# Optimization experiments

Measured on AMD Instinct MI355X. Metric: run time of the kernel, lower is better.

Reference implementation:

```python
import jax, jax.numpy as jnp
import numpy as np

B, T_OUT, L, D, H = 1, 8, 512, 512, 8  # batch, frames, tokens/frame, d_model, heads


def setup_inputs() -> dict:
    key = jax.random.key(0)
    ks = jax.random.split(key, 7)
    return {
        "hidden_states": jax.random.normal(ks[0], (B * T_OUT, L, D), jnp.float32),
        "p_out": jax.random.normal(ks[1], (B, T_OUT, 4, 4), jnp.float32),
        "p_out_inv": jax.random.normal(ks[2], (B, T_OUT, 4, 4), jnp.float32),
        "Wq": jax.random.normal(ks[3], (D, D), jnp.float32) * 0.02,
        "Wk": jax.random.normal(ks[4], (D, D), jnp.float32) * 0.02,
        "Wv": jax.random.normal(ks[5], (D, D), jnp.float32) * 0.02,
        "Wo": jax.random.normal(ks[6], (D, D), jnp.float32) * 0.02,
        "bo": jnp.zeros((D,), jnp.float32),
        "num_heads": H,
    }


def cape_embed(f, P):
    # f: (b, S, d), P: (b, S, 4, 4); rearrange '(d k)'->'d k' with k=4, matmul by P, flatten back
    b, S, d = f.shape
    f4 = f.reshape(b, S, d // 4, 4)
    return jnp.einsum('bsdk,bskg->bsdg', f4, P).reshape(b, S, d)


def reference(hidden_states, p_out, p_out_inv, Wq, Wk, Wv, Wo, bo, num_heads):
    b, t_out = p_out.shape[0], p_out.shape[1]
    bt, l, d = hidden_states.shape
    S = t_out * l
    residual = hidden_states

    # '(b t_out) l d -> b (t_out l) d'
    x = hidden_states.reshape(b, S, d)

    q = x @ Wq
    k = x @ Wk
    v = x @ Wv

    # repeat per-frame CAPE matrices over tokens within each frame; self-attn so p_in = p_out
    Pq = jnp.repeat(p_out_inv, l, axis=1)  # (b, S, 4, 4)
    Pk = jnp.repeat(p_out, l, axis=1)      # (b, S, 4, 4)
    q = cape_embed(q, Pq)
    k = cape_embed(k, Pk)

    hd = d // num_heads
    scale = hd ** -0.5
    qh = q.reshape(b, S, num_heads, hd).transpose(0, 2, 1, 3)  # (b, h, S, hd)
    kh = k.reshape(b, S, num_heads, hd).transpose(0, 2, 1, 3)
    vh = v.reshape(b, S, num_heads, hd).transpose(0, 2, 1, 3)

    scores = jnp.einsum('bhqd,bhkd->bhqk', qh, kh) * scale  # full (b,h,S,S) matrix
    probs = jax.nn.softmax(scores, axis=-1)
    o = jnp.einsum('bhqk,bhkd->bhqd', probs, vh)

    o = o.transpose(0, 2, 1, 3).reshape(b, S, d)
    o = o @ Wo + bo  # to_out[0]; to_out[1] dropout is identity in eval

    # 'b (t_out l) d -> (b t_out) l d'
    o = o.reshape(bt, l, d)
    return o + residual  # residual_connection; rescale_output_factor = 1.0
```

## Files before the change

### kernel.cpp

```cpp
#include <hip/hip_runtime.h>
#include <hip/hip_bf16.h>
#include <stdint.h>

typedef __bf16 bf16_t;
typedef __bf16 bf16x2 __attribute__((ext_vector_type(2)));
typedef __bf16 bf16x4 __attribute__((ext_vector_type(4)));
typedef __bf16 bf16x8 __attribute__((ext_vector_type(8)));
typedef float f32x4 __attribute__((ext_vector_type(4)));

#define MFMA(a, b, c) __builtin_amdgcn_mfma_f32_16x16x32_bf16(a, b, c, 0, 0, 0)

#if __has_builtin(__builtin_amdgcn_exp2f)
#define FEXP2 __builtin_amdgcn_exp2f
#else
#define FEXP2 exp2f
#endif

__device__ __forceinline__ void g2lds16(const void* g, void* l) {
  __builtin_amdgcn_global_load_lds(
      reinterpret_cast<const __attribute__((address_space(1))) unsigned int*>(
          reinterpret_cast<uintptr_t>(g)),
      reinterpret_cast<__attribute__((address_space(3))) unsigned int*>(
          reinterpret_cast<uintptr_t>(l)),
      16, 0, 0);
}

__device__ __forceinline__ unsigned cvtpk(float lo, float hi) {
  unsigned r;
  asm("v_cvt_pk_bf16_f32 %0, %1, %2" : "=v"(r) : "v"(lo), "v"(hi));
  return r;
}

__device__ __forceinline__ void lane_swap32(unsigned& a, unsigned& b) {
#if __has_builtin(__builtin_amdgcn_permlane32_swap)
  typedef int i32x2 __attribute__((ext_vector_type(2)));
  i32x2 r = __builtin_amdgcn_permlane32_swap((int)a, (int)b, false, false);
  a = (unsigned)r[0];
  b = (unsigned)r[1];
#else
  asm("v_permlane32_swap_b32 %0, %1" : "+v"(a), "+v"(b));
#endif
}

__device__ __forceinline__ void lane_swap16(unsigned& a, unsigned& b) {
#if __has_builtin(__builtin_amdgcn_permlane16_swap)
  typedef int i32x2 __attribute__((ext_vector_type(2)));
  i32x2 r = __builtin_amdgcn_permlane16_swap((int)a, (int)b, false, false);
  a = (unsigned)r[0];
  b = (unsigned)r[1];
#else
  asm("v_permlane16_swap_b32 %0, %1" : "+v"(a), "+v"(b));
#endif
}

__global__ __launch_bounds__(256) void k_prep(const float* __restrict__ x,
                                              const float* __restrict__ Wq,
                                              const float* __restrict__ Wk,
                                              const float* __restrict__ Wv,
                                              const float* __restrict__ Wo,
                                              const float* __restrict__ Pout,
                                              const float* __restrict__ Pinv,
                                              bf16_t* __restrict__ Xbf,
                                              bf16_t* __restrict__ WqT,
                                              bf16_t* __restrict__ WkT,
                                              bf16_t* __restrict__ WvT,
                                              bf16_t* __restrict__ WoT) {
  const int bid = blockIdx.x;
  if (bid < 2048) {
    int i = (bid * 256 + threadIdx.x) * 4;
    float4 v = *reinterpret_cast<const float4*>(x + i);
    bf16x4 o;
    o[0] = (bf16_t)v.x; o[1] = (bf16_t)v.y; o[2] = (bf16_t)v.z; o[3] = (bf16_t)v.w;
    *reinterpret_cast<bf16x4*>(Xbf + i) = o;
  } else if (bid < 3072) {
    int idx = (bid - 2048) * 256 + threadIdx.x;
    int t = idx >> 15;
    int n = (idx >> 6) & 511;
    int k0 = (idx & 63) << 3;
    int dq4 = (n >> 2) << 2;
    int g = n & 3;
    float pq[4], pk[4];
#pragma unroll
    for (int h = 0; h < 4; ++h) {
      pq[h] = Pinv[t * 16 + h * 4 + g];
      pk[h] = Pout[t * 16 + h * 4 + g];
    }
    bf16x8 oq, ok;
#pragma unroll
    for (int j = 0; j < 8; ++j) {
      const float4 wq = *reinterpret_cast<const float4*>(Wq + (size_t)(k0 + j) * 512 + dq4);
      const float4 wk = *reinterpret_cast<const float4*>(Wk + (size_t)(k0 + j) * 512 + dq4);
      oq[j] = (bf16_t)((wq.x * pq[0] + wq.y * pq[1] + wq.z * pq[2] + wq.w * pq[3]) * 0.1803368801f);
      ok[j] = (bf16_t)(wk.x * pk[0] + wk.y * pk[1] + wk.z * pk[2] + wk.w * pk[3]);
    }
    size_t o = ((size_t)t * 512 + n) * 512 + k0;
    *reinterpret_cast<bf16x8*>(WqT + o) = oq;
    *reinterpret_cast<bf16x8*>(WkT + o) = ok;
  } else {
    int idx = (bid - 3072) * 256 + threadIdx.x;
    int mat = idx >> 15;
    int n = (idx >> 6) & 511;
    int k0 = (idx & 63) << 3;
    const float* W = mat ? Wo : Wv;
    bf16_t* T = mat ? WoT : WvT;
    bf16x8 o;
#pragma unroll
    for (int j = 0; j < 8; ++j) o[j] = (bf16_t)W[(size_t)(k0 + j) * 512 + n];
    *reinterpret_cast<bf16x8*>(T + (size_t)n * 512 + k0) = o;
  }
}

__global__ __launch_bounds__(256) void k_gemm_qkv(const bf16_t* __restrict__ Xbf,
                                                  const bf16_t* __restrict__ WqT,
                                                  const bf16_t* __restrict__ WkT,
                                                  const bf16_t* __restrict__ WvT,
                                                  bf16_t* __restrict__ Qh,
                                                  bf16_t* __restrict__ Kh,
                                                  bf16_t* __restrict__ Vt) {
  __shared__ bf16_t lA[128 * 64];
  __shared__ bf16_t lB[64 * 64];
  const int m0 = blockIdx.x * 128, n0 = blockIdx.y * 64;
  const int mat = blockIdx.z;
  const int frame = m0 >> 9;
  const bf16_t* WT = (mat == 0) ? (WqT + (size_t)frame * 512 * 512)
                   : (mat == 1) ? (WkT + (size_t)frame * 512 * 512)
                                : WvT;
  const int tid = threadIdx.x, lane = tid & 63, wid = tid >> 6;
  const int wr = wid >> 1, wc = wid & 1;
  const int l15 = lane & 15, lg = lane >> 4;
  const int srow = lane >> 3;
  const int scol = ((lane & 7) ^ (lane >> 3)) << 3;

  f32x4 acc[4][2] = {};

  for (int kt = 0; kt < 512; kt += 64) {
#pragma unroll
    for (int i = 0; i < 4; ++i) {
      int chunk = wid * 4 + i;
      int row = chunk * 8 + srow;
      g2lds16(Xbf + (size_t)(m0 + row) * 512 + kt + scol, lA + chunk * 512);
    }
#pragma unroll
    for (int i = 0; i < 2; ++i) {
      int chunk = wid * 2 + i;
      int row = chunk * 8 + srow;
      g2lds16(WT + (size_t)(n0 + row) * 512 + kt + scol, lB + chunk * 512);
    }
    __syncthreads();
#pragma unroll
    for (int kk = 0; kk < 2; ++kk) {
      bf16x8 af[4], bw[2];
      int c16 = ((4 * kk + lg) ^ (l15 & 7)) << 3;
#pragma unroll
      for (int i = 0; i < 4; ++i)
        af[i] = *reinterpret_cast<const bf16x8*>(lA + (wr * 64 + i * 16 + l15) * 64 + c16);
#pragma unroll
      for (int j = 0; j < 2; ++j)
        bw[j] = *reinterpret_cast<const bf16x8*>(lB + (wc * 32 + j * 16 + l15) * 64 + c16);
#pragma unroll
      for (int i = 0; i < 4; ++i)
#pragma unroll
        for (int j = 0; j < 2; ++j)
          acc[i][j] = MFMA(af[i], bw[j], acc[i][j]);
    }
    __syncthreads();
  }

#pragma unroll
  for (int i = 0; i < 4; ++i)
#pragma unroll
    for (int j = 0; j < 2; ++j)
#pragma unroll
      for (int r = 0; r < 4; ++r) {
        int s = m0 + wr * 64 + i * 16 + lg * 4 + r;
        int n = n0 + wc * 32 + j * 16 + l15;
        bf16_t v = (bf16_t)acc[i][j][r];
        if (mat == 2) {
          Vt[(size_t)n * 4096 + s] = v;
        } else if (mat == 0) {
          Qh[((size_t)(n >> 6) * 4096 + s) * 64 + (n & 63)] = v;
        } else {
          Kh[((size_t)(n >> 6) * 4096 + s) * 64 + (n & 63)] = v;
        }
      }
}

__global__ __launch_bounds__(256, 2) void k_attn(const bf16_t* __restrict__ Qh,
                                                 const bf16_t* __restrict__ Kh,
                                                 const bf16_t* __restrict__ Vt,
                                                 char* __restrict__ wsb,
                                                 float* __restrict__ Lp) {
  __shared__ bf16_t lK[2][64 * 64];
  __shared__ bf16_t lV[2][64 * 64];
  const int h = blockIdx.y;
  const int ks = blockIdx.z;
  const int q0 = blockIdx.x * 256;
  const int tid = threadIdx.x, lane = tid & 63, wid = tid >> 6;
  const int l15 = lane & 15, lg = lane >> 4;
  const int srow = lane >> 3;
  const int scol = ((lane & 7) ^ (lane >> 3)) << 3;

  bf16_t* Op = (bf16_t*)(ks < 3 ? wsb + ((size_t)ks << 22) : wsb + (29u << 20));

  bf16x8 qf[4][2];
#pragma unroll
  for (int g = 0; g < 4; ++g) {
    const bf16_t* Qp = Qh + ((size_t)h * 4096 + q0 + wid * 64 + g * 16 + l15) * 64;
#pragma unroll
    for (int kk = 0; kk < 2; ++kk)
      qf[g][kk] = *reinterpret_cast<const bf16x8*>(Qp + kk * 32 + lg * 8);
  }

  bf16x8 onesf;
#pragma unroll
  for (int j = 0; j < 8; ++j) onesf[j] = (bf16_t)1.0f;

  const bf16_t* Kb = Kh + ((size_t)h * 4096 + ks * 1024) * 64;
  const bf16_t* Vb = Vt + (size_t)h * 64 * 4096 + ks * 1024;

  f32x4 oT[4][4] = {};
  f32x4 lac[4] = {};

  auto stage = [&](int buf, int kt) {
#pragma unroll
    for (int i = 0; i < 2; ++i) {
      int chunk = wid * 2 + i;
      int row = chunk * 8 + srow;
      g2lds16(Kb + (size_t)(kt + row) * 64 + scol, &lK[buf][chunk * 512]);
      g2lds16(Vb + (size_t)row * 4096 + kt + scol, &lV[buf][chunk * 512]);
    }
  };

  stage(0, 0);
  __syncthreads();

  for (int t = 0; t < 16; ++t) {
    const int cur = t & 1;
    if (t < 15) stage(cur ^ 1, (t + 1) * 64);

    f32x4 st[4][4] = {};
    __builtin_amdgcn_s_setprio(1);
#pragma unroll
    for (int kk = 0; kk < 2; ++kk)
#pragma unroll
      for (int mb = 0; mb < 4; ++mb) {
        bf16x8 kf = *reinterpret_cast<const bf16x8*>(
            &lK[cur][(mb * 16 + l15) * 64 + (((kk * 4 + lg) ^ (l15 & 7)) << 3)]);
        st[0][mb] = MFMA(kf, qf[0][kk], st[0][mb]);
        st[1][mb] = MFMA(kf, qf[1][kk], st[1][mb]);
        st[2][mb] = MFMA(kf, qf[2][kk], st[2][mb]);
        st[3][mb] = MFMA(kf, qf[3][kk], st[3][mb]);
      }
    __builtin_amdgcn_s_setprio(0);

#pragma unroll
    for (int g = 0; g < 4; ++g)
#pragma unroll
      for (int mb = 0; mb < 4; ++mb)
#pragma unroll
        for (int r = 0; r < 4; ++r)
          st[g][mb][r] = FEXP2(st[g][mb][r]);

    bf16x8 pb[4][2];
#pragma unroll
    for (int g = 0; g < 4; ++g)
#pragma unroll
      for (int kk = 0; kk < 2; ++kk) {
        unsigned A  = cvtpk(st[g][2 * kk][0],     st[g][2 * kk][1]);
        unsigned Ap = cvtpk(st[g][2 * kk][2],     st[g][2 * kk][3]);
        unsigned B  = cvtpk(st[g][2 * kk + 1][0], st[g][2 * kk + 1][1]);
        unsigned Bp = cvtpk(st[g][2 * kk + 1][2], st[g][2 * kk + 1][3]);
        lane_swap32(A, B);
        lane_swap16(A, B);
        lane_swap32(Ap, Bp);
        lane_swap16(Ap, Bp);
        union { unsigned u[4]; bf16x8 v; } pu;
        pu.u[0] = A; pu.u[1] = Ap; pu.u[2] = B; pu.u[3] = Bp;
        pb[g][kk] = pu.v;
      }

    __builtin_amdgcn_s_setprio(1);
#pragma unroll
    for (int kk = 0; kk < 2; ++kk) {
      lac[0] = MFMA(onesf, pb[0][kk], lac[0]);
      lac[1] = MFMA(onesf, pb[1][kk], lac[1]);
      lac[2] = MFMA(onesf, pb[2][kk], lac[2]);
      lac[3] = MFMA(onesf, pb[3][kk], lac[3]);
#pragma unroll
      for (int hb = 0; hb < 4; ++hb) {
        bf16x8 vf = *reinterpret_cast<const bf16x8*>(
            &lV[cur][(hb * 16 + l15) * 64 + (((kk * 4 + lg) ^ (l15 & 7)) << 3)]);
        oT[0][hb] = MFMA(vf, pb[0][kk], oT[0][hb]);
        oT[1][hb] = MFMA(vf, pb[1][kk], oT[1][hb]);
        oT[2][hb] = MFMA(vf, pb[2][kk], oT[2][hb]);
        oT[3][hb] = MFMA(vf, pb[3][kk], oT[3][hb]);
      }
    }
    __builtin_amdgcn_s_setprio(0);
    __syncthreads();
  }

#pragma unroll
  for (int g = 0; g < 4; ++g) {
    int q = q0 + wid * 64 + g * 16 + l15;
    size_t rbase = ((size_t)ks * 8 + h) * 4096 + q;
    size_t obase = ((size_t)h * 4096 + q) * 64;
    if (lg == 0) Lp[rbase] = lac[g][0];
#pragma unroll
    for (int hb = 0; hb < 4; ++hb) {
      bf16x4 ov;
#pragma unroll
      for (int r = 0; r < 4; ++r) ov[r] = (bf16_t)oT[g][hb][r];
      *reinterpret_cast<bf16x4*>(Op + obase + hb * 16 + lg * 4) = ov;
    }
  }
}

__global__ __launch_bounds__(256) void k_merge(char* __restrict__ wsb,
                                               const float* __restrict__ Lp,
                                               bf16_t* __restrict__ Obf) {
  int idx = blockIdx.x * 256 + threadIdx.x;
  int d4 = (idx & 15) << 2;
  int row = idx >> 4;
  float l = 0.f;
  f32x4 o = {};
#pragma unroll
  for (int s = 0; s < 4; ++s) {
    const bf16_t* Ops = (const bf16_t*)(s < 3 ? wsb + ((size_t)s << 22) : wsb + (29u << 20));
    l += Lp[s * 32768 + row];
    bf16x4 v = *reinterpret_cast<const bf16x4*>(Ops + (size_t)row * 64 + d4);
    o[0] += (float)v[0]; o[1] += (float)v[1];
    o[2] += (float)v[2]; o[3] += (float)v[3];
  }
  float rinv = 1.f / l;
  int h = row >> 12, q = row & 4095;
  bf16x4 ov;
#pragma unroll
  for (int r = 0; r < 4; ++r) ov[r] = (bf16_t)(o[r] * rinv);
  *reinterpret_cast<bf16x4*>(Obf + (size_t)q * 512 + h * 64 + d4) = ov;
}

__global__ __launch_bounds__(256) void k_gemm_out(const bf16_t* __restrict__ Obf,
                                                  const bf16_t* __restrict__ WoT,
                                                  const float* __restrict__ bo,
                                                  const float* __restrict__ resid,
                                                  float* __restrict__ out) {
  __shared__ bf16_t lA[64 * 64];
  __shared__ bf16_t lB[64 * 64];
  const int m0 = blockIdx.x * 64, n0 = blockIdx.y * 64;
  const int tid = threadIdx.x, lane = tid & 63, wid = tid >> 6;
  const int wr = wid >> 1, wc = wid & 1;
  const int l15 = lane & 15, lg = lane >> 4;
  const int srow = lane >> 3;
  const int scol = ((lane & 7) ^ (lane >> 3)) << 3;

  f32x4 acc[2][2] = {};

  for (int kt = 0; kt < 512; kt += 64) {
#pragma unroll
    for (int i = 0; i < 2; ++i) {
      int chunk = wid * 2 + i;
      int row = chunk * 8 + srow;
      g2lds16(Obf + (size_t)(m0 + row) * 512 + kt + scol, lA + chunk * 512);
      g2lds16(WoT + (size_t)(n0 + row) * 512 + kt + scol, lB + chunk * 512);
    }
    __syncthreads();
#pragma unroll
    for (int kk = 0; kk < 2; ++kk) {
      bf16x8 af[2], bw[2];
      int c16 = ((4 * kk + lg) ^ (l15 & 7)) << 3;
#pragma unroll
      for (int i = 0; i < 2; ++i) {
        af[i] = *reinterpret_cast<const bf16x8*>(lA + (wr * 32 + i * 16 + l15) * 64 + c16);
        bw[i] = *reinterpret_cast<const bf16x8*>(lB + (wc * 32 + i * 16 + l15) * 64 + c16);
      }
#pragma unroll
      for (int i = 0; i < 2; ++i)
#pragma unroll
        for (int j = 0; j < 2; ++j)
          acc[i][j] = MFMA(af[i], bw[j], acc[i][j]);
    }
    __syncthreads();
  }

#pragma unroll
  for (int i = 0; i < 2; ++i)
#pragma unroll
    for (int j = 0; j < 2; ++j)
#pragma unroll
      for (int r = 0; r < 4; ++r) {
        int s = m0 + wr * 32 + i * 16 + lg * 4 + r;
        int n = n0 + wc * 32 + j * 16 + l15;
        size_t o = (size_t)s * 512 + n;
        out[o] = acc[i][j][r] + bo[n] + resid[o];
      }
}

extern "C" void kernel_launch(void* const* d_in, const int* in_sizes, int n_in,
                              void* d_out, int out_size, void* d_ws, size_t ws_size,
                              hipStream_t stream) {
  const float* hs   = (const float*)d_in[0];
  const float* pout = (const float*)d_in[1];
  const float* pinv = (const float*)d_in[2];
  const float* Wq   = (const float*)d_in[3];
  const float* Wk   = (const float*)d_in[4];
  const float* Wv   = (const float*)d_in[5];
  const float* Wo   = (const float*)d_in[6];
  const float* bo   = (const float*)d_in[7];
  float* out = (float*)d_out;

  char* ws = (char*)d_ws;
  bf16_t* Xbf = (bf16_t*)(ws);
  bf16_t* WqT = (bf16_t*)(ws + (4u << 20));
  bf16_t* WkT = (bf16_t*)(ws + (8u << 20));
  bf16_t* WvT = (bf16_t*)(ws + (12u << 20));
  bf16_t* WoT = (bf16_t*)(ws + (12u << 20) + (512u << 10));
  bf16_t* Qh  = (bf16_t*)(ws + (13u << 20));
  bf16_t* Kh  = (bf16_t*)(ws + (17u << 20));
  bf16_t* Vt  = (bf16_t*)(ws + (21u << 20));
  bf16_t* Obf = (bf16_t*)(ws + (25u << 20));
  float*  Lp  = (float*)(ws + (33u << 20));

  hipLaunchKernelGGL(k_prep, dim3(3328), dim3(256), 0, stream,
                     hs, Wq, Wk, Wv, Wo, pout, pinv, Xbf, WqT, WkT, WvT, WoT);
  hipLaunchKernelGGL(k_gemm_qkv, dim3(32, 8, 3), dim3(256), 0, stream,
                     Xbf, WqT, WkT, WvT, Qh, Kh, Vt);
  hipLaunchKernelGGL(k_attn, dim3(16, 8, 4), dim3(256), 0, stream, Qh, Kh, Vt, ws, Lp);
  hipLaunchKernelGGL(k_merge, dim3(2048), dim3(256), 0, stream, ws, Lp, Obf);
  hipLaunchKernelGGL(k_gemm_out, dim3(64, 8), dim3(256), 0, stream, Obf, WoT, bo, hs, out);
}
```

Before: 93.76 us.

## Fuse split-K attention merge into output GEMM and widen QKV GEMM tile

Removes the separate k_merge kernel. The output-projection GEMM now sums the four split-K partial outputs, normalizes them by the summed row sums, and writes the merged bf16 A tile straight into LDS, so the Obf round trip and one launch go away. The QKV GEMM tile grows from 128x64 to 128x128, which halves the grid and improves per-block operand reuse. The trade-off is that each of the 8 column blocks of the out GEMM recomputes the merge for its rows, giving redundant partial-O reads. The larger QKV tile also gives fewer blocks, which may fill the CUs less evenly.

```diff
diff --git a/kernel.cpp b/kernel.cpp
--- a/kernel.cpp
+++ b/kernel.cpp
@@ -118,8 +118,8 @@
                                                   bf16_t* __restrict__ Kh,
                                                   bf16_t* __restrict__ Vt) {
   __shared__ bf16_t lA[128 * 64];
-  __shared__ bf16_t lB[64 * 64];
-  const int m0 = blockIdx.x * 128, n0 = blockIdx.y * 64;
+  __shared__ bf16_t lB[128 * 64];
+  const int m0 = blockIdx.x * 128, n0 = blockIdx.y * 128;
   const int mat = blockIdx.z;
   const int frame = m0 >> 9;
   const bf16_t* WT = (mat == 0) ? (WqT + (size_t)frame * 512 * 512)
@@ -131,7 +131,7 @@
   const int srow = lane >> 3;
   const int scol = ((lane & 7) ^ (lane >> 3)) << 3;
 
-  f32x4 acc[4][2] = {};
+  f32x4 acc[4][4] = {};
 
   for (int kt = 0; kt < 512; kt += 64) {
 #pragma unroll
@@ -139,28 +139,24 @@
       int chunk = wid * 4 + i;
       int row = chunk * 8 + srow;
       g2lds16(Xbf + (size_t)(m0 + row) * 512 + kt + scol, lA + chunk * 512);
-    }
-#pragma unroll
-    for (int i = 0; i < 2; ++i) {
-      int chunk = wid * 2 + i;
-      int row = chunk * 8 + srow;
       g2lds16(WT + (size_t)(n0 + row) * 512 + kt + scol, lB + chunk * 512);
     }
     __syncthreads();
 #pragma unroll
     for (int kk = 0; kk < 2; ++kk) {
-      bf16x8 af[4], bw[2];
-      int c16 = ((4 * kk + lg) ^ (l15 & 7)) << 3;
+      bf16x8 af[4], bw[4];
+#pragma unroll
+      for (int i = 0; i < 4; ++i) {
+        int ar = wr * 64 + i * 16 + l15;
+        int br = wc * 64 + i * 16 + l15;
+        int c16 = ((4 * kk + lg) ^ (l15 & 7)) << 3;
+        af[i] = *reinterpret_cast<const bf16x8*>(lA + ar * 64 + c16);
+        bw[i] = *reinterpret_cast<const bf16x8*>(lB + br * 64 + c16);
+      }
 #pragma unroll
       for (int i = 0; i < 4; ++i)
-        af[i] = *reinterpret_cast<const bf16x8*>(lA + (wr * 64 + i * 16 + l15) * 64 + c16);
-#pragma unroll
-      for (int j = 0; j < 2; ++j)
-        bw[j] = *reinterpret_cast<const bf16x8*>(lB + (wc * 32 + j * 16 + l15) * 64 + c16);
-#pragma unroll
-      for (int i = 0; i < 4; ++i)
-#pragma unroll
-        for (int j = 0; j < 2; ++j)
+#pragma unroll
+        for (int j = 0; j < 4; ++j)
           acc[i][j] = MFMA(af[i], bw[j], acc[i][j]);
     }
     __syncthreads();
@@ -169,11 +165,11 @@
 #pragma unroll
   for (int i = 0; i < 4; ++i)
 #pragma unroll
-    for (int j = 0; j < 2; ++j)
+    for (int j = 0; j < 4; ++j)
 #pragma unroll
       for (int r = 0; r < 4; ++r) {
         int s = m0 + wr * 64 + i * 16 + lg * 4 + r;
-        int n = n0 + wc * 32 + j * 16 + l15;
+        int n = n0 + wc * 64 + j * 16 + l15;
         bf16_t v = (bf16_t)acc[i][j][r];
         if (mat == 2) {
           Vt[(size_t)n * 4096 + s] = v;
@@ -316,31 +312,8 @@
   }
 }
 
-__global__ __launch_bounds__(256) void k_merge(char* __restrict__ wsb,
-                                               const float* __restrict__ Lp,
-                                               bf16_t* __restrict__ Obf) {
-  int idx = blockIdx.x * 256 + threadIdx.x;
-  int d4 = (idx & 15) << 2;
-  int row = idx >> 4;
-  float l = 0.f;
-  f32x4 o = {};
-#pragma unroll
-  for (int s = 0; s < 4; ++s) {
-    const bf16_t* Ops = (const bf16_t*)(s < 3 ? wsb + ((size_t)s << 22) : wsb + (29u << 20));
-    l += Lp[s * 32768 + row];
-    bf16x4 v = *reinterpret_cast<const bf16x4*>(Ops + (size_t)row * 64 + d4);
-    o[0] += (float)v[0]; o[1] += (float)v[1];
-    o[2] += (float)v[2]; o[3] += (float)v[3];
-  }
-  float rinv = 1.f / l;
-  int h = row >> 12, q = row & 4095;
-  bf16x4 ov;
-#pragma unroll
-  for (int r = 0; r < 4; ++r) ov[r] = (bf16_t)(o[r] * rinv);
-  *reinterpret_cast<bf16x4*>(Obf + (size_t)q * 512 + h * 64 + d4) = ov;
-}
-
-__global__ __launch_bounds__(256) void k_gemm_out(const bf16_t* __restrict__ Obf,
+__global__ __launch_bounds__(256) void k_gemm_out(char* __restrict__ wsb,
+                                                  const float* __restrict__ Lp,
                                                   const bf16_t* __restrict__ WoT,
                                                   const float* __restrict__ bo,
                                                   const float* __restrict__ resid,
@@ -354,15 +327,38 @@
   const int srow = lane >> 3;
   const int scol = ((lane & 7) ^ (lane >> 3)) << 3;
 
+  const bf16_t* Op0 = (const bf16_t*)(wsb);
+  const bf16_t* Op1 = (const bf16_t*)(wsb + (1u << 22));
+  const bf16_t* Op2 = (const bf16_t*)(wsb + (2u << 22));
+  const bf16_t* Op3 = (const bf16_t*)(wsb + (29u << 20));
+
   f32x4 acc[2][2] = {};
 
   for (int kt = 0; kt < 512; kt += 64) {
+    const int h = kt >> 6;
 #pragma unroll
     for (int i = 0; i < 2; ++i) {
       int chunk = wid * 2 + i;
       int row = chunk * 8 + srow;
-      g2lds16(Obf + (size_t)(m0 + row) * 512 + kt + scol, lA + chunk * 512);
       g2lds16(WoT + (size_t)(n0 + row) * 512 + kt + scol, lB + chunk * 512);
+    }
+#pragma unroll
+    for (int i = 0; i < 2; ++i) {
+      int chunk = wid * 2 + i;
+      int q = m0 + chunk * 8 + srow;
+      size_t rb = (size_t)h * 4096 + q;
+      float l = ((Lp[rb] + Lp[32768 + rb]) + Lp[65536 + rb]) + Lp[98304 + rb];
+      float rinv = 1.f / l;
+      size_t ob = rb * 64 + scol;
+      bf16x8 v0 = *reinterpret_cast<const bf16x8*>(Op0 + ob);
+      bf16x8 v1 = *reinterpret_cast<const bf16x8*>(Op1 + ob);
+      bf16x8 v2 = *reinterpret_cast<const bf16x8*>(Op2 + ob);
+      bf16x8 v3 = *reinterpret_cast<const bf16x8*>(Op3 + ob);
+      bf16x8 m8;
+#pragma unroll
+      for (int j = 0; j < 8; ++j)
+        m8[j] = (bf16_t)(((((float)v0[j] + (float)v1[j]) + (float)v2[j]) + (float)v3[j]) * rinv);
+      *reinterpret_cast<bf16x8*>(lA + chunk * 512 + lane * 8) = m8;
     }
     __syncthreads();
 #pragma unroll
@@ -418,14 +414,13 @@
   bf16_t* Qh  = (bf16_t*)(ws + (13u << 20));
   bf16_t* Kh  = (bf16_t*)(ws + (17u << 20));
   bf16_t* Vt  = (bf16_t*)(ws + (21u << 20));
-  bf16_t* Obf = (bf16_t*)(ws + (25u << 20));
   float*  Lp  = (float*)(ws + (33u << 20));
 
   hipLaunchKernelGGL(k_prep, dim3(3328), dim3(256), 0, stream,
                      hs, Wq, Wk, Wv, Wo, pout, pinv, Xbf, WqT, WkT, WvT, WoT);
-  hipLaunchKernelGGL(k_gemm_qkv, dim3(32, 8, 3), dim3(256), 0, stream,
+  hipLaunchKernelGGL(k_gemm_qkv, dim3(32, 4, 3), dim3(256), 0, stream,
                      Xbf, WqT, WkT, WvT, Qh, Kh, Vt);
   hipLaunchKernelGGL(k_attn, dim3(16, 8, 4), dim3(256), 0, stream, Qh, Kh, Vt, ws, Lp);
-  hipLaunchKernelGGL(k_merge, dim3(2048), dim3(256), 0, stream, ws, Lp, Obf);
-  hipLaunchKernelGGL(k_gemm_out, dim3(64, 8), dim3(256), 0, stream, Obf, WoT, bo, hs, out);
-}
+  hipLaunchKernelGGL(k_gemm_out, dim3(64, 8), dim3(256), 0, stream,
+                     ws, Lp, WoT, bo, hs, out);
+}
```

Result: slower. 99.05 us (+5.6%).

## Fuse split-K attention merge into attention kernel via last-block atomic counter

Applied to the files above, without the earlier changes.

Removes the separate k_merge launch. Each attention block fences its partial output and bumps a per-(head, query-tile) atomic counter, and the fourth block to arrive sums the four partials and normalizes them into Obf. The counters are zeroed in k_prep. This saves one kernel launch and its gap, but serializes the merge onto the last-arriving block of each tile and adds fences and an atomic.

```diff
diff --git a/kernel.cpp b/kernel.cpp
--- a/kernel.cpp
+++ b/kernel.cpp
@@ -64,8 +64,10 @@
                                               bf16_t* __restrict__ WqT,
                                               bf16_t* __restrict__ WkT,
                                               bf16_t* __restrict__ WvT,
-                                              bf16_t* __restrict__ WoT) {
+                                              bf16_t* __restrict__ WoT,
+                                              int* __restrict__ cnt) {
   const int bid = blockIdx.x;
+  if (bid == 0 && threadIdx.x < 128) cnt[threadIdx.x] = 0;
   if (bid < 2048) {
     int i = (bid * 256 + threadIdx.x) * 4;
     float4 v = *reinterpret_cast<const float4*>(x + i);
@@ -189,9 +191,12 @@
                                                  const bf16_t* __restrict__ Kh,
                                                  const bf16_t* __restrict__ Vt,
                                                  char* __restrict__ wsb,
-                                                 float* __restrict__ Lp) {
+                                                 float* __restrict__ Lp,
+                                                 int* __restrict__ cnt,
+                                                 bf16_t* __restrict__ Obf) {
   __shared__ bf16_t lK[2][64 * 64];
   __shared__ bf16_t lV[2][64 * 64];
+  __shared__ int winner;
   const int h = blockIdx.y;
   const int ks = blockIdx.z;
   const int q0 = blockIdx.x * 256;
@@ -314,30 +319,35 @@
       *reinterpret_cast<bf16x4*>(Op + obase + hb * 16 + lg * 4) = ov;
     }
   }
-}
-
-__global__ __launch_bounds__(256) void k_merge(char* __restrict__ wsb,
-                                               const float* __restrict__ Lp,
-                                               bf16_t* __restrict__ Obf) {
-  int idx = blockIdx.x * 256 + threadIdx.x;
-  int d4 = (idx & 15) << 2;
-  int row = idx >> 4;
-  float l = 0.f;
-  f32x4 o = {};
-#pragma unroll
-  for (int s = 0; s < 4; ++s) {
-    const bf16_t* Ops = (const bf16_t*)(s < 3 ? wsb + ((size_t)s << 22) : wsb + (29u << 20));
-    l += Lp[s * 32768 + row];
-    bf16x4 v = *reinterpret_cast<const bf16x4*>(Ops + (size_t)row * 64 + d4);
-    o[0] += (float)v[0]; o[1] += (float)v[1];
-    o[2] += (float)v[2]; o[3] += (float)v[3];
-  }
-  float rinv = 1.f / l;
-  int h = row >> 12, q = row & 4095;
-  bf16x4 ov;
-#pragma unroll
-  for (int r = 0; r < 4; ++r) ov[r] = (bf16_t)(o[r] * rinv);
-  *reinterpret_cast<bf16x4*>(Obf + (size_t)q * 512 + h * 64 + d4) = ov;
+
+  __threadfence();
+  if (tid == 0) winner = (atomicAdd(&cnt[h * 16 + blockIdx.x], 1) == 3);
+  __syncthreads();
+  if (winner) {
+    __threadfence();
+    const bf16_t* O0 = (const bf16_t*)(wsb);
+    const bf16_t* O1 = (const bf16_t*)(wsb + (1u << 22));
+    const bf16_t* O2 = (const bf16_t*)(wsb + (2u << 22));
+    const bf16_t* O3 = (const bf16_t*)(wsb + (29u << 20));
+    for (int it = tid; it < 4096; it += 256) {
+      int r = it >> 4;
+      int d4 = (it & 15) << 2;
+      int q = q0 + r;
+      size_t row = (size_t)h * 4096 + q;
+      float l = ((Lp[row] + Lp[32768 + row]) + Lp[65536 + row]) + Lp[98304 + row];
+      size_t ob = row * 64 + d4;
+      bf16x4 v0 = *reinterpret_cast<const bf16x4*>(O0 + ob);
+      bf16x4 v1 = *reinterpret_cast<const bf16x4*>(O1 + ob);
+      bf16x4 v2 = *reinterpret_cast<const bf16x4*>(O2 + ob);
+      bf16x4 v3 = *reinterpret_cast<const bf16x4*>(O3 + ob);
+      float rinv = 1.f / l;
+      bf16x4 ov;
+#pragma unroll
+      for (int j = 0; j < 4; ++j)
+        ov[j] = (bf16_t)((((((float)v0[j] + (float)v1[j]) + (float)v2[j]) + (float)v3[j])) * rinv);
+      *reinterpret_cast<bf16x4*>(Obf + (size_t)q * 512 + h * 64 + d4) = ov;
+    }
+  }
 }
 
 __global__ __launch_bounds__(256) void k_gemm_out(const bf16_t* __restrict__ Obf,
@@ -420,12 +430,13 @@
   bf16_t* Vt  = (bf16_t*)(ws + (21u << 20));
   bf16_t* Obf = (bf16_t*)(ws + (25u << 20));
   float*  Lp  = (float*)(ws + (33u << 20));
+  int*    cnt = (int*)(ws + (33u << 20) + (768u << 10));
 
   hipLaunchKernelGGL(k_prep, dim3(3328), dim3(256), 0, stream,
-                     hs, Wq, Wk, Wv, Wo, pout, pinv, Xbf, WqT, WkT, WvT, WoT);
+                     hs, Wq, Wk, Wv, Wo, pout, pinv, Xbf, WqT, WkT, WvT, WoT, cnt);
   hipLaunchKernelGGL(k_gemm_qkv, dim3(32, 8, 3), dim3(256), 0, stream,
                      Xbf, WqT, WkT, WvT, Qh, Kh, Vt);
-  hipLaunchKernelGGL(k_attn, dim3(16, 8, 4), dim3(256), 0, stream, Qh, Kh, Vt, ws, Lp);
-  hipLaunchKernelGGL(k_merge, dim3(2048), dim3(256), 0, stream, ws, Lp, Obf);
+  hipLaunchKernelGGL(k_attn, dim3(16, 8, 4), dim3(256), 0, stream,
+                     Qh, Kh, Vt, ws, Lp, cnt, Obf);
   hipLaunchKernelGGL(k_gemm_out, dim3(64, 8), dim3(256), 0, stream, Obf, WoT, bo, hs, out);
 }
```

Result: slower. 162.4 us (+73.2%).
